# Kernel tuning notes

Measured on AMD Instinct MI355X. Metric: run time of the kernel, lower is better.

Reference implementation:

```python
import jax, jax.numpy as jnp
import numpy as np
import math

D_MODEL = 1024
N_HEADS = 16
D_K = D_MODEL // N_HEADS
HIDDEN = 4096
R_SOFTPLUS_0 = 1.442695041
EPS = 1e-6


def setup_inputs() -> dict:
    key = jax.random.key(0)
    ks = jax.random.split(key, 16)
    B, S = 4, 2048
    s = 0.02
    inp = {
        "inputs": jax.random.normal(ks[0], (B, S, D_MODEL), jnp.float32),
        "mask": jnp.zeros((1, 1, S, S), jnp.float32),
        # RmsNorm (direct_scale=True -> init 1.0)
        "rms_scale": jnp.ones((D_MODEL,), jnp.float32),
        # attention projections (torch Linear: y = x @ W.T + b)
        "Wq": jax.random.normal(ks[1], (D_MODEL, D_MODEL), jnp.float32) * s,
        "bq": jnp.zeros((D_MODEL,), jnp.float32),
        "Wk": jax.random.normal(ks[2], (D_MODEL, D_MODEL), jnp.float32) * s,
        "bk": jnp.zeros((D_MODEL,), jnp.float32),
        "Wv": jax.random.normal(ks[3], (D_MODEL, D_MODEL), jnp.float32) * s,
        "bv": jnp.zeros((D_MODEL,), jnp.float32),
        "per_dim_scale": jnp.zeros((D_K,), jnp.float32),
        "Wpost": jax.random.normal(ks[4], (D_MODEL, D_MODEL), jnp.float32) * s,
        "bpost": jnp.zeros((D_MODEL,), jnp.float32),
        # FFN LayerNorm (direct_scale=False -> scale param init 0, effective 1+scale)
        "ln_scale": jnp.zeros((D_MODEL,), jnp.float32),
        "ln_bias": jnp.zeros((D_MODEL,), jnp.float32),
        "W1": jax.random.normal(ks[5], (HIDDEN, D_MODEL), jnp.float32) * s,
        "b1": jnp.zeros((HIDDEN,), jnp.float32),
        "W2": jax.random.normal(ks[6], (D_MODEL, HIDDEN), jnp.float32) * s,
        "b2": jnp.zeros((D_MODEL,), jnp.float32),
    }
    return inp


def _rms_norm(x, scale):
    ms = jnp.mean(x * x, axis=-1, keepdims=True)
    return x * jax.lax.rsqrt(ms + EPS) * scale


def _layer_norm(x, scale, bias):
    mean = jnp.mean(x, axis=-1, keepdims=True)
    var = jnp.mean((x - mean) ** 2, axis=-1, keepdims=True)
    return (x - mean) * jax.lax.rsqrt(var + EPS) * (1.0 + scale) + bias


def reference(inputs, mask, rms_scale, Wq, bq, Wk, bk, Wv, bv, per_dim_scale,
              Wpost, bpost, ln_scale, ln_bias, W1, b1, W2, b2):
    B, S, _ = inputs.shape
    x = _rms_norm(inputs, rms_scale)
    # projections -> [B, H, S, Dk]
    def split_heads(t):
        return t.reshape(B, S, N_HEADS, D_K).transpose(0, 2, 1, 3)
    q = split_heads(x @ Wq.T + bq)
    k = split_heads(x @ Wk.T + bk)
    v = split_heads(x @ Wv.T + bv)
    # PerDimScale: (r_softplus_0 / sqrt(d_k)) * softplus(param)
    scale = (R_SOFTPLUS_0 / math.sqrt(D_K)) * jax.nn.softplus(per_dim_scale)
    q = q * scale
    attn = jnp.einsum("bhqd,bhkd->bhqk", q, k) + mask
    attn = jax.nn.softmax(attn, axis=-1)
    out = jnp.einsum("bhqk,bhkd->bhqd", attn, v)
    out = out.transpose(0, 2, 1, 3).reshape(B, S, D_MODEL)
    attn_out = out @ Wpost.T + bpost
    h = attn_out + inputs  # residual (dropout=0)
    # FeedForward with pre-LayerNorm and residual
    y = _layer_norm(h, ln_scale, ln_bias)
    y = jax.nn.relu(y @ W1.T + b1)
    y = y @ W2.T + b2
    return y + h
```

## Files before the change

### kernel.cpp

```cpp
#include <hip/hip_runtime.h>
#include <hip/hip_bf16.h>

typedef unsigned short u16;
typedef __attribute__((ext_vector_type(8))) short short8;
typedef __attribute__((ext_vector_type(4))) float floatx4;

#define R_PDS 0.18033688f
#define LOG2E 1.4426950408889634f

__device__ __forceinline__ float bf2f(u16 u) {
    union { float f; unsigned int i; } c; c.i = ((unsigned int)u) << 16; return c.f;
}
__device__ __forceinline__ u16 f2b(float f) {
    union { float f; unsigned int i; } c; c.f = f;
    unsigned int r = c.i + 0x7fffu + ((c.i >> 16) & 1u);
    return (u16)(r >> 16);
}
__device__ __forceinline__ unsigned int pk2(float a, float b) {
    __hip_bfloat162 h = __float22bfloat162_rn(float2{a, b});
    unsigned int u; __builtin_memcpy(&u, &h, 4); return u;
}

__device__ __forceinline__ void async16(const u16* g, u16* l) {
    __builtin_amdgcn_global_load_lds(
        (const __attribute__((address_space(1))) unsigned int*)g,
        (__attribute__((address_space(3))) unsigned int*)l, 16, 0, 0);
}

__global__ __launch_bounds__(256) void f2b_all_k(const float* __restrict__ Wq, const float* __restrict__ Wk,
                                                 const float* __restrict__ Wv, const float* __restrict__ Wp,
                                                 const float* __restrict__ W1, const float* __restrict__ W2,
                                                 u16* __restrict__ Wqkvb, u16* __restrict__ Wpb,
                                                 u16* __restrict__ W1b,  u16* __restrict__ W2b,
                                                 int* flag) {
    int bid = blockIdx.x;
    if (bid == 0 && threadIdx.x == 0) *flag = 0;
    const float* src; u16* dst; int off;
    if      (bid < 1024) { src = Wq; dst = Wqkvb;                off = bid; }
    else if (bid < 2048) { src = Wk; dst = Wqkvb + 1024 * 1024;  off = bid - 1024; }
    else if (bid < 3072) { src = Wv; dst = Wqkvb + 2048 * 1024;  off = bid - 2048; }
    else if (bid < 4096) { src = Wp; dst = Wpb;                  off = bid - 3072; }
    else if (bid < 8192) { src = W1; dst = W1b;                  off = bid - 4096; }
    else                 { src = W2; dst = W2b;                  off = bid - 8192; }
    int i = off * 256 + threadIdx.x;
    float4 v = ((const float4*)src)[i];
    uint2 w; w.x = pk2(v.x, v.y); w.y = pk2(v.z, v.w);
    ((uint2*)dst)[i] = w;
}

__global__ __launch_bounds__(256) void mask_any_k(const float* __restrict__ mask, int* flag) {
    int i = blockIdx.x * 256 + threadIdx.x;
    uint4 u = ((const uint4*)mask)[i];
    unsigned int v = (u.x | u.y | u.z | u.w) & 0x7fffffffu;
    if (v) atomicOr(flag, 1);
}

__global__ __launch_bounds__(256) void rmsnorm_k(const float* __restrict__ in,
                                                 const float* __restrict__ gscale,
                                                 u16* __restrict__ out) {
    int row = blockIdx.x;
    int t = threadIdx.x, lane = t & 63, wave = t >> 6;
    const float* x = in + (size_t)row * 1024;
    float4 v = *(const float4*)(x + t * 4);
    float ss = v.x*v.x + v.y*v.y + v.z*v.z + v.w*v.w;
    for (int o = 1; o < 64; o <<= 1) ss += __shfl_xor(ss, o, 64);
    __shared__ float red[4];
    if (lane == 0) red[wave] = ss;
    __syncthreads();
    float tot = red[0] + red[1] + red[2] + red[3];
    float inv = rsqrtf(tot * (1.0f / 1024.0f) + 1e-6f);
    float4 s = *(const float4*)(gscale + t * 4);
    uint2 w;
    w.x = pk2(v.x * inv * s.x, v.y * inv * s.y);
    w.y = pk2(v.z * inv * s.z, v.w * inv * s.w);
    *(uint2*)(out + (size_t)row * 1024 + t * 4) = w;
}

__global__ __launch_bounds__(256) void layernorm_k(const u16* __restrict__ in,
                                                   const float* __restrict__ gs,
                                                   const float* __restrict__ gb,
                                                   u16* __restrict__ out) {
    int row = blockIdx.x;
    int t = threadIdx.x, lane = t & 63, wave = t >> 6;
    const u16* x = in + (size_t)row * 1024;
    uint2 u = *(const uint2*)(x + t * 4);
    float v0 = bf2f((u16)(u.x & 0xffff)), v1 = bf2f((u16)(u.x >> 16));
    float v2 = bf2f((u16)(u.y & 0xffff)), v3 = bf2f((u16)(u.y >> 16));
    float s1 = v0 + v1 + v2 + v3;
    float s2 = v0*v0 + v1*v1 + v2*v2 + v3*v3;
    for (int o = 1; o < 64; o <<= 1) { s1 += __shfl_xor(s1, o, 64); s2 += __shfl_xor(s2, o, 64); }
    __shared__ float r1[4], r2[4];
    if (lane == 0) { r1[wave] = s1; r2[wave] = s2; }
    __syncthreads();
    float mean = (r1[0] + r1[1] + r1[2] + r1[3]) * (1.0f / 1024.0f);
    float var  = (r2[0] + r2[1] + r2[2] + r2[3]) * (1.0f / 1024.0f) - mean * mean;
    var = fmaxf(var, 0.0f);
    float inv = rsqrtf(var + 1e-6f);
    float4 sc = *(const float4*)(gs + t * 4);
    float4 bb = *(const float4*)(gb + t * 4);
    uint2 w;
    w.x = pk2((v0 - mean) * inv * (1.0f + sc.x) + bb.x,
              (v1 - mean) * inv * (1.0f + sc.y) + bb.y);
    w.y = pk2((v2 - mean) * inv * (1.0f + sc.z) + bb.z,
              (v3 - mean) * inv * (1.0f + sc.w) + bb.w);
    *(uint2*)(out + (size_t)row * 1024 + t * 4) = w;
}

template <int EPI, bool OUTF32, bool RESF32>
__global__ __launch_bounds__(256) void gemm_bt_k(const u16* __restrict__ A,
                                                 const u16* __restrict__ B,
                                                 const float* __restrict__ bias,
                                                 const void* __restrict__ res,
                                                 void* __restrict__ Cv,
                                                 int M, int N, int K) {
    __shared__ __align__(16) u16 As[4096];
    __shared__ __align__(16) u16 Bs[4096];
    const int t = threadIdx.x, wave = t >> 6, lane = t & 63;
    const int quad = lane >> 4, ln = lane & 15;
    const int m0 = blockIdx.y * 128, n0 = blockIdx.x * 128;
    const int wm = (wave >> 1) * 64, wn = (wave & 1) * 64;

    floatx4 acc[4][4];
    for (int mt = 0; mt < 4; mt++) for (int nt = 0; nt < 4; nt++) acc[mt][nt] = (floatx4)0.0f;

    const int c0 = t, c1 = t + 256;
    const u16* Ap0 = A + (size_t)(m0 + (c0 >> 2)) * K + (c0 & 3) * 8;
    const u16* Ap1 = A + (size_t)(m0 + (c1 >> 2)) * K + (c1 & 3) * 8;
    const u16* Bp0 = B + (size_t)(n0 + (c0 >> 2)) * K + (c0 & 3) * 8;
    const u16* Bp1 = B + (size_t)(n0 + (c1 >> 2)) * K + (c1 & 3) * 8;
    u16* AsW0 = As + wave * 512;
    u16* AsW1 = As + 2048 + wave * 512;
    u16* BsW0 = Bs + wave * 512;
    u16* BsW1 = Bs + 2048 + wave * 512;

    for (int kt = 0; kt < K; kt += 32) {
        __syncthreads();
        async16(Ap0 + kt, AsW0);
        async16(Ap1 + kt, AsW1);
        async16(Bp0 + kt, BsW0);
        async16(Bp1 + kt, BsW1);
        __syncthreads();
        short8 af[4], bfr[4];
        for (int mt = 0; mt < 4; mt++)
            af[mt] = *(const short8*)&As[(wm + mt * 16 + ln) * 32 + quad * 8];
        for (int nt = 0; nt < 4; nt++)
            bfr[nt] = *(const short8*)&Bs[(wn + nt * 16 + ln) * 32 + quad * 8];
        for (int mt = 0; mt < 4; mt++)
            for (int nt = 0; nt < 4; nt++)
                acc[mt][nt] = __builtin_amdgcn_mfma_f32_16x16x32_bf16(af[mt], bfr[nt], acc[mt][nt], 0, 0, 0);
    }

    for (int nt = 0; nt < 4; nt++) {
        int col = n0 + wn + nt * 16 + ln;
        float bv = bias[col];
        for (int mt = 0; mt < 4; mt++) {
            for (int r = 0; r < 4; r++) {
                int row = m0 + wm + mt * 16 + quad * 4 + r;
                float v = acc[mt][nt][r] + bv;
                if (EPI == 1) v = fmaxf(v, 0.0f);
                if (EPI == 2) {
                    if (RESF32) v += ((const float*)res)[(size_t)row * N + col];
                    else        v += bf2f(((const u16*)res)[(size_t)row * N + col]);
                }
                if (OUTF32) ((float*)Cv)[(size_t)row * N + col] = v;
                else        ((u16*)Cv)[(size_t)row * N + col] = f2b(v);
            }
        }
    }
}

__global__ __launch_bounds__(256) void gemm_qkv_k(const u16* __restrict__ A,
                                                  const u16* __restrict__ B,
                                                  const float* __restrict__ bq,
                                                  const float* __restrict__ bk,
                                                  const float* __restrict__ bv,
                                                  const float* __restrict__ pds,
                                                  u16* __restrict__ C) {
    const int K = 1024, N = 3072;
    __shared__ __align__(16) u16 As[4096];
    __shared__ __align__(16) u16 Bs[4096];
    const int t = threadIdx.x, wave = t >> 6, lane = t & 63;
    const int quad = lane >> 4, ln = lane & 15;
    const int m0 = blockIdx.y * 128, n0 = blockIdx.x * 128;
    const int wm = (wave >> 1) * 64, wn = (wave & 1) * 64;

    floatx4 acc[4][4];
    for (int mt = 0; mt < 4; mt++) for (int nt = 0; nt < 4; nt++) acc[mt][nt] = (floatx4)0.0f;

    const int c0 = t, c1 = t + 256;
    const u16* Ap0 = A + (size_t)(m0 + (c0 >> 2)) * K + (c0 & 3) * 8;
    const u16* Ap1 = A + (size_t)(m0 + (c1 >> 2)) * K + (c1 & 3) * 8;
    const u16* Bp0 = B + (size_t)(n0 + (c0 >> 2)) * K + (c0 & 3) * 8;
    const u16* Bp1 = B + (size_t)(n0 + (c1 >> 2)) * K + (c1 & 3) * 8;
    u16* AsW0 = As + wave * 512;
    u16* AsW1 = As + 2048 + wave * 512;
    u16* BsW0 = Bs + wave * 512;
    u16* BsW1 = Bs + 2048 + wave * 512;

    for (int kt = 0; kt < K; kt += 32) {
        __syncthreads();
        async16(Ap0 + kt, AsW0);
        async16(Ap1 + kt, AsW1);
        async16(Bp0 + kt, BsW0);
        async16(Bp1 + kt, BsW1);
        __syncthreads();
        short8 af[4], bfr[4];
        for (int mt = 0; mt < 4; mt++)
            af[mt] = *(const short8*)&As[(wm + mt * 16 + ln) * 32 + quad * 8];
        for (int nt = 0; nt < 4; nt++)
            bfr[nt] = *(const short8*)&Bs[(wn + nt * 16 + ln) * 32 + quad * 8];
        for (int mt = 0; mt < 4; mt++)
            for (int nt = 0; nt < 4; nt++)
                acc[mt][nt] = __builtin_amdgcn_mfma_f32_16x16x32_bf16(af[mt], bfr[nt], acc[mt][nt], 0, 0, 0);
    }

    for (int nt = 0; nt < 4; nt++) {
        int col = n0 + wn + nt * 16 + ln;
        float bv_, sc = 1.0f;
        if (col < 1024) {
            bv_ = bq[col];
            float xp = pds[col & 63];
            float sp = (xp > 20.0f) ? xp : log1pf(__expf(xp));
            sc = R_PDS * sp * LOG2E;
        } else if (col < 2048) bv_ = bk[col - 1024];
        else                   bv_ = bv[col - 2048];
        for (int mt = 0; mt < 4; mt++)
            for (int r = 0; r < 4; r++) {
                int row = m0 + wm + mt * 16 + quad * 4 + r;
                C[(size_t)row * N + col] = f2b((acc[mt][nt][r] + bv_) * sc);
            }
    }
}

__global__ __launch_bounds__(256) void transpose_v_k(const u16* __restrict__ qkv, u16* __restrict__ vT) {
    __shared__ u16 tile[64][65];
    int st = blockIdx.x, bh = blockIdx.y;
    int b = bh >> 4, h = bh & 15;
    const u16* vb = qkv + (size_t)(b * 2048 + st * 64) * 3072 + 2048 + h * 64;
    int t = threadIdx.x;
    for (int i = t; i < 4096; i += 256) {
        int s = i >> 6, d = i & 63;
        tile[s][d] = vb[(size_t)s * 3072 + d];
    }
    __syncthreads();
    u16* ob = vT + (size_t)bh * 131072 + st * 64;
    for (int i = t; i < 4096; i += 256) {
        int d = i >> 6, s = i & 63;
        ob[(size_t)d * 2048 + s] = tile[s][d];
    }
}

__global__ __launch_bounds__(256) void attn_k(const u16* __restrict__ qkv,
                                              const u16* __restrict__ vT,
                                              const float* __restrict__ mask,
                                              const int* __restrict__ flag,
                                              u16* __restrict__ o) {
    __shared__ __align__(16) u16 QPs[64][72];
    __shared__ __align__(16) u16 Ks[64][72];
    __shared__ __align__(16) u16 Vs[64][72];

    const int t = threadIdx.x, wave = t >> 6, lane = t & 63;
    const int quad = lane >> 4, ln = lane & 15;
    const int qt = blockIdx.x, bh = blockIdx.y;
    const int b = bh >> 4, h = bh & 15;
    const int q0 = qt * 64;

    const u16* qb = qkv + (size_t)(b * 2048 + q0) * 3072 + h * 64;
    for (int c = t; c < 512; c += 256) {
        int row = c >> 3, seg = c & 7;
        *(uint4*)&QPs[row][seg * 8] = *(const uint4*)(qb + (size_t)row * 3072 + seg * 8);
    }
    __syncthreads();

    short8 qf[2];
    for (int ks = 0; ks < 2; ks++)
        qf[ks] = *(const short8*)&QPs[wave * 16 + ln][ks * 32 + quad * 8];

    short8 ones_f;
    for (int i = 0; i < 8; i++) ones_f[i] = (short)0x3F80;

    floatx4 acc_o[4], acc_l = (floatx4)0.0f;
    for (int dt = 0; dt < 4; dt++) acc_o[dt] = (floatx4)0.0f;

    const int mflag = *flag;
    const u16* kb = qkv + (size_t)(b * 2048) * 3072 + 1024 + h * 64;
    const u16* vg = vT + (size_t)bh * 131072;

    const int r0 = t >> 3, s0 = (t & 7) * 8;
    const u16* kp0 = kb + (size_t)r0 * 3072 + s0;
    const u16* kp1 = kb + (size_t)(r0 + 32) * 3072 + s0;
    const u16* vp0 = vg + (size_t)r0 * 2048 + s0;
    const u16* vp1 = vg + (size_t)(r0 + 32) * 2048 + s0;

    uint4 kr0 = *(const uint4*)(kp0);
    uint4 kr1 = *(const uint4*)(kp1);
    uint4 vr0 = *(const uint4*)(vp0);
    uint4 vr1 = *(const uint4*)(vp1);

    for (int kv0 = 0; kv0 < 2048; kv0 += 64) {
        __syncthreads();
        *(uint4*)&Ks[r0][s0]      = kr0;
        *(uint4*)&Ks[r0 + 32][s0] = kr1;
        *(uint4*)&Vs[r0][s0]      = vr0;
        *(uint4*)&Vs[r0 + 32][s0] = vr1;
        __syncthreads();
        if (kv0 + 64 < 2048) {
            size_t ko = (size_t)(kv0 + 64) * 3072;
            int    vo = kv0 + 64;
            kr0 = *(const uint4*)(kp0 + ko);
            kr1 = *(const uint4*)(kp1 + ko);
            vr0 = *(const uint4*)(vp0 + vo);
            vr1 = *(const uint4*)(vp1 + vo);
        }

        floatx4 acc_s[4];
        for (int nt = 0; nt < 4; nt++) acc_s[nt] = (floatx4)0.0f;
        for (int ks = 0; ks < 2; ks++)
            for (int nt = 0; nt < 4; nt++) {
                short8 bfr = *(const short8*)&Ks[nt * 16 + ln][ks * 32 + quad * 8];
                acc_s[nt] = __builtin_amdgcn_mfma_f32_16x16x32_bf16(qf[ks], bfr, acc_s[nt], 0, 0, 0);
            }
        if (mflag) {
            for (int nt = 0; nt < 4; nt++)
                for (int r = 0; r < 4; r++) {
                    int qr = q0 + wave * 16 + quad * 4 + r;
                    int kc = kv0 + nt * 16 + ln;
                    acc_s[nt][r] += mask[(size_t)qr * 2048 + kc] * LOG2E;
                }
        }

        int prow = wave * 16 + quad * 4;
        for (int nt = 0; nt < 4; nt++) {
            unsigned int u01 = pk2(__builtin_amdgcn_exp2f(fminf(acc_s[nt][0], 80.0f)),
                                   __builtin_amdgcn_exp2f(fminf(acc_s[nt][1], 80.0f)));
            unsigned int u23 = pk2(__builtin_amdgcn_exp2f(fminf(acc_s[nt][2], 80.0f)),
                                   __builtin_amdgcn_exp2f(fminf(acc_s[nt][3], 80.0f)));
            QPs[prow + 0][nt * 16 + ln] = (u16)(u01 & 0xffff);
            QPs[prow + 1][nt * 16 + ln] = (u16)(u01 >> 16);
            QPs[prow + 2][nt * 16 + ln] = (u16)(u23 & 0xffff);
            QPs[prow + 3][nt * 16 + ln] = (u16)(u23 >> 16);
        }

        for (int ks = 0; ks < 2; ks++) {
            short8 a = *(const short8*)&QPs[wave * 16 + ln][ks * 32 + quad * 8];
            acc_l = __builtin_amdgcn_mfma_f32_16x16x32_bf16(a, ones_f, acc_l, 0, 0, 0);
            for (int dt = 0; dt < 4; dt++) {
                short8 bfr = *(const short8*)&Vs[dt * 16 + ln][ks * 32 + quad * 8];
                acc_o[dt] = __builtin_amdgcn_mfma_f32_16x16x32_bf16(a, bfr, acc_o[dt], 0, 0, 0);
            }
        }
    }

    u16* ob = o + (size_t)(b * 2048 + q0) * 1024 + h * 64;
    for (int r = 0; r < 4; r++) {
        float inv = 1.0f / acc_l[r];
        int row = wave * 16 + quad * 4 + r;
        for (int dt = 0; dt < 4; dt++)
            ob[(size_t)row * 1024 + dt * 16 + ln] = f2b(acc_o[dt][r] * inv);
    }
}

extern "C" void kernel_launch(void* const* d_in, const int* in_sizes, int n_in,
                              void* d_out, int out_size, void* d_ws, size_t ws_size,
                              hipStream_t stream) {
    const float* inp    = (const float*)d_in[0];
    const float* mask   = (const float*)d_in[1];
    const float* rms_s  = (const float*)d_in[2];
    const float* Wq     = (const float*)d_in[3];
    const float* bq     = (const float*)d_in[4];
    const float* Wk     = (const float*)d_in[5];
    const float* bk     = (const float*)d_in[6];
    const float* Wv     = (const float*)d_in[7];
    const float* bv     = (const float*)d_in[8];
    const float* pds    = (const float*)d_in[9];
    const float* Wpost  = (const float*)d_in[10];
    const float* bpost  = (const float*)d_in[11];
    const float* ln_s   = (const float*)d_in[12];
    const float* ln_b   = (const float*)d_in[13];
    const float* W1     = (const float*)d_in[14];
    const float* b1     = (const float*)d_in[15];
    const float* W2     = (const float*)d_in[16];
    const float* b2     = (const float*)d_in[17];
    float* out = (float*)d_out;

    char* w = (char*)d_ws;
    const size_t MB = 1u << 20;
    u16* W1b   = (u16*)(w + 0 * MB);
    u16* W2b   = (u16*)(w + 8 * MB);
    u16* qkv   = (u16*)(w + 16 * MB);
    u16* x     = (u16*)(w + 64 * MB);
    u16* o     = (u16*)(w + 64 * MB);
    u16* Wqkvb = (u16*)(w + 80 * MB);
    u16* Wpb   = (u16*)(w + 86 * MB);
    u16* yln   = (u16*)(w + 80 * MB);
    u16* vT    = (u16*)(w + 96 * MB);
    u16* hb    = (u16*)(w + 96 * MB);
    u16* f1    = (u16*)(w + 16 * MB);
    int* flag  = (int*)(w + 112 * MB);

    f2b_all_k<<<12288, 256, 0, stream>>>(Wq, Wk, Wv, Wpost, W1, W2, Wqkvb, Wpb, W1b, W2b, flag);
    mask_any_k<<<4096, 256, 0, stream>>>(mask, flag);

    rmsnorm_k<<<8192, 256, 0, stream>>>(inp, rms_s, x);

    gemm_qkv_k<<<dim3(24, 64), 256, 0, stream>>>(x, Wqkvb, bq, bk, bv, pds, qkv);

    transpose_v_k<<<dim3(32, 64), 256, 0, stream>>>(qkv, vT);

    attn_k<<<dim3(32, 64), 256, 0, stream>>>(qkv, vT, mask, flag, o);

    gemm_bt_k<2, false, true><<<dim3(8, 64), 256, 0, stream>>>(o, Wpb, bpost, inp, hb, 8192, 1024, 1024);

    layernorm_k<<<8192, 256, 0, stream>>>(hb, ln_s, ln_b, yln);

    gemm_bt_k<1, false, true><<<dim3(32, 64), 256, 0, stream>>>(yln, W1b, b1, nullptr, f1, 8192, 4096, 1024);
    gemm_bt_k<2, true, false><<<dim3(8, 64), 256, 0, stream>>>(f1, W2b, b2, hb, out, 8192, 1024, 4096);
}
```

Before: 609.8 us.

## Double attention query tile to 128 rows per block with two M-tiles per wave

Each attention block now handles 128 query rows instead of 64, and each wave processes two 16-row M-tiles. Every K/V tile loaded into shared memory is therefore reused across twice as many queries, halving K/V global traffic and the number of block-level syncs per query. The QK^T product is computed transposed (K as the A operand), so each lane holds four consecutive key columns and can write P to shared memory with one packed 64-bit store instead of four scalar stores. The cost is more registers per thread, a larger shared buffer, and half as many blocks (1024), which may lower occupancy and latency hiding.

```diff
diff --git a/kernel.cpp b/kernel.cpp
--- a/kernel.cpp
+++ b/kernel.cpp
@@ -255,7 +255,7 @@
                                               const float* __restrict__ mask,
                                               const int* __restrict__ flag,
                                               u16* __restrict__ o) {
-    __shared__ __align__(16) u16 QPs[64][72];
+    __shared__ __align__(16) u16 QPs[128][72];
     __shared__ __align__(16) u16 Ks[64][72];
     __shared__ __align__(16) u16 Vs[64][72];
 
@@ -263,24 +263,29 @@
     const int quad = lane >> 4, ln = lane & 15;
     const int qt = blockIdx.x, bh = blockIdx.y;
     const int b = bh >> 4, h = bh & 15;
-    const int q0 = qt * 64;
+    const int q0 = qt * 128;
+    const int wm = wave * 32;
 
     const u16* qb = qkv + (size_t)(b * 2048 + q0) * 3072 + h * 64;
-    for (int c = t; c < 512; c += 256) {
+    for (int c = t; c < 1024; c += 256) {
         int row = c >> 3, seg = c & 7;
         *(uint4*)&QPs[row][seg * 8] = *(const uint4*)(qb + (size_t)row * 3072 + seg * 8);
     }
     __syncthreads();
 
-    short8 qf[2];
-    for (int ks = 0; ks < 2; ks++)
-        qf[ks] = *(const short8*)&QPs[wave * 16 + ln][ks * 32 + quad * 8];
+    short8 qf[2][2];
+    for (int mt = 0; mt < 2; mt++)
+        for (int ks = 0; ks < 2; ks++)
+            qf[mt][ks] = *(const short8*)&QPs[wm + mt * 16 + ln][ks * 32 + quad * 8];
 
     short8 ones_f;
     for (int i = 0; i < 8; i++) ones_f[i] = (short)0x3F80;
 
-    floatx4 acc_o[4], acc_l = (floatx4)0.0f;
-    for (int dt = 0; dt < 4; dt++) acc_o[dt] = (floatx4)0.0f;
+    floatx4 acc_o[2][4], acc_l[2];
+    for (int mt = 0; mt < 2; mt++) {
+        acc_l[mt] = (floatx4)0.0f;
+        for (int dt = 0; dt < 4; dt++) acc_o[mt][dt] = (floatx4)0.0f;
+    }
 
     const int mflag = *flag;
     const u16* kb = qkv + (size_t)(b * 2048) * 3072 + 1024 + h * 64;
@@ -313,50 +318,59 @@
             vr1 = *(const uint4*)(vp1 + vo);
         }
 
-        floatx4 acc_s[4];
-        for (int nt = 0; nt < 4; nt++) acc_s[nt] = (floatx4)0.0f;
-        for (int ks = 0; ks < 2; ks++)
-            for (int nt = 0; nt < 4; nt++) {
-                short8 bfr = *(const short8*)&Ks[nt * 16 + ln][ks * 32 + quad * 8];
-                acc_s[nt] = __builtin_amdgcn_mfma_f32_16x16x32_bf16(qf[ks], bfr, acc_s[nt], 0, 0, 0);
-            }
-        if (mflag) {
-            for (int nt = 0; nt < 4; nt++)
+        for (int nt = 0; nt < 4; nt++) {
+            floatx4 sa0 = (floatx4)0.0f, sa1 = (floatx4)0.0f;
+            for (int ks = 0; ks < 2; ks++) {
+                short8 kf = *(const short8*)&Ks[nt * 16 + ln][ks * 32 + quad * 8];
+                sa0 = __builtin_amdgcn_mfma_f32_16x16x32_bf16(kf, qf[0][ks], sa0, 0, 0, 0);
+                sa1 = __builtin_amdgcn_mfma_f32_16x16x32_bf16(kf, qf[1][ks], sa1, 0, 0, 0);
+            }
+            if (mflag) {
                 for (int r = 0; r < 4; r++) {
-                    int qr = q0 + wave * 16 + quad * 4 + r;
-                    int kc = kv0 + nt * 16 + ln;
-                    acc_s[nt][r] += mask[(size_t)qr * 2048 + kc] * LOG2E;
+                    int kc = kv0 + nt * 16 + quad * 4 + r;
+                    sa0[r] += mask[(size_t)(q0 + wm + ln) * 2048 + kc] * LOG2E;
+                    sa1[r] += mask[(size_t)(q0 + wm + 16 + ln) * 2048 + kc] * LOG2E;
                 }
+            }
+            {
+                uint2 w;
+                w.x = pk2(__builtin_amdgcn_exp2f(fminf(sa0[0], 80.0f)),
+                          __builtin_amdgcn_exp2f(fminf(sa0[1], 80.0f)));
+                w.y = pk2(__builtin_amdgcn_exp2f(fminf(sa0[2], 80.0f)),
+                          __builtin_amdgcn_exp2f(fminf(sa0[3], 80.0f)));
+                *(uint2*)&QPs[wm + ln][nt * 16 + quad * 4] = w;
+            }
+            {
+                uint2 w;
+                w.x = pk2(__builtin_amdgcn_exp2f(fminf(sa1[0], 80.0f)),
+                          __builtin_amdgcn_exp2f(fminf(sa1[1], 80.0f)));
+                w.y = pk2(__builtin_amdgcn_exp2f(fminf(sa1[2], 80.0f)),
+                          __builtin_amdgcn_exp2f(fminf(sa1[3], 80.0f)));
+                *(uint2*)&QPs[wm + 16 + ln][nt * 16 + quad * 4] = w;
+            }
         }
 
-        int prow = wave * 16 + quad * 4;
-        for (int nt = 0; nt < 4; nt++) {
-            unsigned int u01 = pk2(__builtin_amdgcn_exp2f(fminf(acc_s[nt][0], 80.0f)),
-                                   __builtin_amdgcn_exp2f(fminf(acc_s[nt][1], 80.0f)));
-            unsigned int u23 = pk2(__builtin_amdgcn_exp2f(fminf(acc_s[nt][2], 80.0f)),
-                                   __builtin_amdgcn_exp2f(fminf(acc_s[nt][3], 80.0f)));
-            QPs[prow + 0][nt * 16 + ln] = (u16)(u01 & 0xffff);
-            QPs[prow + 1][nt * 16 + ln] = (u16)(u01 >> 16);
-            QPs[prow + 2][nt * 16 + ln] = (u16)(u23 & 0xffff);
-            QPs[prow + 3][nt * 16 + ln] = (u16)(u23 >> 16);
-        }
-
         for (int ks = 0; ks < 2; ks++) {
-            short8 a = *(const short8*)&QPs[wave * 16 + ln][ks * 32 + quad * 8];
-            acc_l = __builtin_amdgcn_mfma_f32_16x16x32_bf16(a, ones_f, acc_l, 0, 0, 0);
+            short8 a0 = *(const short8*)&QPs[wm + ln][ks * 32 + quad * 8];
+            short8 a1 = *(const short8*)&QPs[wm + 16 + ln][ks * 32 + quad * 8];
+            acc_l[0] = __builtin_amdgcn_mfma_f32_16x16x32_bf16(a0, ones_f, acc_l[0], 0, 0, 0);
+            acc_l[1] = __builtin_amdgcn_mfma_f32_16x16x32_bf16(a1, ones_f, acc_l[1], 0, 0, 0);
             for (int dt = 0; dt < 4; dt++) {
                 short8 bfr = *(const short8*)&Vs[dt * 16 + ln][ks * 32 + quad * 8];
-                acc_o[dt] = __builtin_amdgcn_mfma_f32_16x16x32_bf16(a, bfr, acc_o[dt], 0, 0, 0);
+                acc_o[0][dt] = __builtin_amdgcn_mfma_f32_16x16x32_bf16(a0, bfr, acc_o[0][dt], 0, 0, 0);
+                acc_o[1][dt] = __builtin_amdgcn_mfma_f32_16x16x32_bf16(a1, bfr, acc_o[1][dt], 0, 0, 0);
             }
         }
     }
 
     u16* ob = o + (size_t)(b * 2048 + q0) * 1024 + h * 64;
-    for (int r = 0; r < 4; r++) {
-        float inv = 1.0f / acc_l[r];
-        int row = wave * 16 + quad * 4 + r;
-        for (int dt = 0; dt < 4; dt++)
-            ob[(size_t)row * 1024 + dt * 16 + ln] = f2b(acc_o[dt][r] * inv);
+    for (int mt = 0; mt < 2; mt++) {
+        for (int r = 0; r < 4; r++) {
+            float inv = 1.0f / acc_l[mt][r];
+            int row = wm + mt * 16 + quad * 4 + r;
+            for (int dt = 0; dt < 4; dt++)
+                ob[(size_t)row * 1024 + dt * 16 + ln] = f2b(acc_o[mt][dt][r] * inv);
+        }
     }
 }
 
@@ -407,7 +421,7 @@
 
     transpose_v_k<<<dim3(32, 64), 256, 0, stream>>>(qkv, vT);
 
-    attn_k<<<dim3(32, 64), 256, 0, stream>>>(qkv, vT, mask, flag, o);
+    attn_k<<<dim3(16, 64), 256, 0, stream>>>(qkv, vT, mask, flag, o);
 
     gemm_bt_k<2, false, true><<<dim3(8, 64), 256, 0, stream>>>(o, Wpb, bpost, inp, hb, 8192, 1024, 1024);
 
```

Result: faster. 594.7 us (-2.5%).
